# Performance work log

Measured on AMD Instinct MI355X. Metric: run time of the kernel, lower is better.

Reference implementation:

```python
import jax, jax.numpy as jnp
import numpy as np

V = 20000   # token vocab (num_embeddings)
SC = 4000   # sub-char vocab (new_size of sub_char embedding)
D = 128     # embedding_dim
L = 15      # max nodes per decomposition tree (<= 8 leaves)
B, S = 32, 512


def _build_trees(rng):
    """Random binary decomposition trees in topological order (children < parent)."""
    node_ids = np.zeros((V, L), np.int32)
    left = np.full((V, L), -1, np.int32)
    right = np.full((V, L), -1, np.int32)
    last = np.zeros((V,), np.int32)
    for v in range(V):
        n_leaves = int(rng.integers(2, 9))
        stack, nodes = [], []
        leaves_left = n_leaves
        while leaves_left > 0 or len(stack) > 1:
            if leaves_left > 0 and (len(stack) < 2 or rng.random() < 0.5):
                nodes.append((-1, -1)); leaves_left -= 1
            else:
                r = stack.pop(); l = stack.pop()
                nodes.append((l, r))
            stack.append(len(nodes) - 1)
        n = len(nodes)
        for j, (l, r) in enumerate(nodes):
            left[v, j] = l; right[v, j] = r
        node_ids[v, :n] = rng.integers(0, SC, n)
        last[v] = n - 1
    return node_ids, left, right, last


def setup_inputs() -> dict:
    key = jax.random.key(0)
    k1, k2, k3, k4 = jax.random.split(key, 4)
    rng = np.random.default_rng(0)
    node_ids, left, right, last = _build_trees(rng)
    inp = {
        "input": jax.random.randint(k1, (B, S), 0, V, dtype=jnp.int32),
        "node_ids": jnp.asarray(node_ids),
        "left": jnp.asarray(left),
        "right": jnp.asarray(right),
        "last": jnp.asarray(last),
        "emb": jax.random.normal(k2, (SC, 5 * D), jnp.float32) * 0.1,   # sub_char weights
        "Wlh_w": jax.random.normal(k3, (D, 5 * D), jnp.float32) * 0.05,  # Linear(D,5D), x @ W
        "Wlh_b": jnp.zeros((5 * D,), jnp.float32),
        "Wrh_w": jax.random.normal(k4, (D, 5 * D), jnp.float32) * 0.05,
        "Wrh_b": jnp.zeros((5 * D,), jnp.float32),
    }
    return inp


def _tree_lstm(node_ids, left, right, last, emb, Wlh_w, Wlh_b, Wrh_w, Wrh_b):
    nV, nL = node_ids.shape
    gv = jnp.arange(nV)

    def step(carry, xs):
        h_all, c_all = carry                  # [V, L, D] each
        ids, l, r, j = xs                     # [V], [V], [V], scalar
        is_int = (l >= 0)[:, None]            # internal node mask; leaf has l==r==-1
        li, ri = jnp.maximum(l, 0), jnp.maximum(r, 0)
        hl, hr = h_all[gv, li], h_all[gv, ri]  # gather children states [V, D]
        cl, cr = c_all[gv, li], c_all[gv, ri]
        s = emb[ids]                           # [V, 5D]
        s_int = s + (hl @ Wlh_w + Wlh_b) + (hr @ Wrh_w + Wrh_b)
        s = jnp.where(is_int, s_int, s)
        ig, lfg, rfg, og, ug = jnp.split(s, 5, axis=1)
        c = jax.nn.sigmoid(ig) * jnp.tanh(ug)
        c = c + jnp.where(is_int, jax.nn.sigmoid(lfg) * cl + jax.nn.sigmoid(rfg) * cr, 0.0)
        h = jax.nn.sigmoid(og) * jnp.tanh(c)
        h_all = h_all.at[:, j].set(h)
        c_all = c_all.at[:, j].set(c)
        return (h_all, c_all), None

    init = (jnp.zeros((nV, nL, emb.shape[1] // 5), emb.dtype),
            jnp.zeros((nV, nL, emb.shape[1] // 5), emb.dtype))
    xs = (node_ids.T, left.T, right.T, jnp.arange(nL))
    (h_all, _), _ = jax.lax.scan(step, init, xs)
    return h_all[gv, last]                     # root h per vocab entry [V, D]


def reference(input, node_ids, left, right, last, emb, Wlh_w, Wlh_b, Wrh_w, Wrh_b):
    lut = _tree_lstm(node_ids, left, right, last, emb, Wlh_w, Wlh_b, Wrh_w, Wrh_b)  # [V, D]
    return lut[input]                          # [B, S, D]
```

## Files before the change

### kernel.cpp

```cpp
#include <hip/hip_runtime.h>
#include <hip/hip_fp16.h>
#include <math.h>

#define V    20000
#define SCV  4000
#define LL   15
#define OUTN (16384 * 128)

#define LEAF_BIT 0x40000000
#define REF_MASK 0x3FFFFFFF
#define ROOT_BIT 0x20000000
#define SLOT_MASK 0x1FFFFFFF
#define DUMMY_SLOT 89999

#define OFF_COUNTS 0
#define OFF_ROOT   128
#define OFF_LISTS  80384
#define OFF_LEAFH  3920384
#define OFF_LEAFC  5968384
#define OFF_LEAFHH 8016384
#define OFF_LT     9040384
#define OFF_RT     14160384
#define OFF_WT     19280384
#define OFF_BIAS   19608064
#define OFF_HINT   19610624
#define OFF_CINT   65690624
#define OFF_HH     111770624
#define OFF_USED   134810624

__device__ __constant__ int d_listOff[8] = {0, 0, 80000, 120000, 160000, 180000, 200000, 220000};

#define ROUND_BLOCKS 256
#define H1_BLOCKS    1920

typedef _Float16 f16x8 __attribute__((ext_vector_type(8)));
typedef float    f32x4 __attribute__((ext_vector_type(4)));

__device__ __forceinline__ float sigm(float x) { return 1.0f / (1.0f + expf(-x)); }

__global__ void mark_kernel(const int* __restrict__ input, unsigned char* __restrict__ used) {
    int i = blockIdx.x * 256 + threadIdx.x;
    used[input[i]] = 1;
}

__global__ void leaf_kernel(const float* __restrict__ emb,
                            float* __restrict__ leafH, float* __restrict__ leafC,
                            __half* __restrict__ leafHh) {
    int row = blockIdx.x;
    int i   = threadIdx.x;
    const float* e = emb + row * 640;
    float ig = e[i];
    float og = e[384 + i];
    float ug = e[512 + i];
    float c = sigm(ig) * tanhf(ug);
    float h = sigm(og) * tanhf(c);
    leafH[row * 128 + i] = h;
    leafC[row * 128 + i] = c;
    leafHh[row * 128 + i] = __float2half(h);
}

__launch_bounds__(320)
__global__ void table_kernel(const float* __restrict__ leafH,
                             const float* __restrict__ Wl, const float* __restrict__ Wlb,
                             const float* __restrict__ Wr, const float* __restrict__ Wrb,
                             __half* __restrict__ LT, __half* __restrict__ RT) {
    __shared__ float A[16 * 128];
    int which = blockIdx.y;
    const float* W  = which ? Wr : Wl;
    const float* Wb = which ? Wrb : Wlb;
    __half* OUT     = which ? RT : LT;
    int r0 = blockIdx.x * 16;
    int t = threadIdx.x;
    for (int idx = t; idx < 16 * 128; idx += 320) A[idx] = leafH[r0 * 128 + idx];
    float acc0[16], acc1[16];
    float b0 = Wb[2 * t], b1 = Wb[2 * t + 1];
#pragma unroll
    for (int m = 0; m < 16; ++m) { acc0[m] = b0; acc1[m] = b1; }
    __syncthreads();
    const float* Bp = W + 2 * t;
#pragma unroll 1
    for (int kb = 0; kb < 128; kb += 4) {
        float4 a[16];
#pragma unroll
        for (int m = 0; m < 16; ++m) a[m] = *(const float4*)(A + (m << 7) + kb);
        float2 bb[4];
#pragma unroll
        for (int u = 0; u < 4; ++u) bb[u] = *(const float2*)(Bp + (kb + u) * 640);
#pragma unroll
        for (int u = 0; u < 4; ++u)
#pragma unroll
            for (int m = 0; m < 16; ++m) {
                float av = (&a[m].x)[u];
                acc0[m] = fmaf(av, bb[u].x, acc0[m]);
                acc1[m] = fmaf(av, bb[u].y, acc1[m]);
            }
    }
#pragma unroll
    for (int m = 0; m < 16; ++m)
        ((__half2*)OUT)[(r0 + m) * 320 + t] = __float22half2_rn(make_float2(acc0[m], acc1[m]));
}

__global__ void wt_kernel(const float* __restrict__ Wl, const float* __restrict__ Wr,
                          __half* __restrict__ WT) {
    __shared__ float T[64][65];
    int kb = blockIdx.x * 64, nb = blockIdx.y * 64;
    int tx = threadIdx.x & 63, ty = threadIdx.x >> 6;
    for (int kk = ty; kk < 64; kk += 4) {
        int k = kb + kk;
        const float* Wsrc = (k < 128) ? (Wl + k * 640) : (Wr + (k - 128) * 640);
        T[kk][tx] = Wsrc[nb + tx];
    }
    __syncthreads();
    for (int nn = ty; nn < 64; nn += 4)
        WT[(nb + nn) * 256 + kb + tx] = __float2half(T[tx][nn]);
}

__global__ void bias_kernel(const float* __restrict__ Wlb, const float* __restrict__ Wrb,
                            float* __restrict__ biasSum) {
    int i = threadIdx.x;
    biasSum[i] = Wlb[i] + Wrb[i];
}

#define MT 128
__global__ void meta_kernel(const int* __restrict__ node_ids,
                            const int* __restrict__ left,
                            const int* __restrict__ right,
                            const int* __restrict__ last,
                            const unsigned char* __restrict__ used,
                            int* __restrict__ counts,
                            int* __restrict__ rootSlot,
                            int4* __restrict__ lists) {
    __shared__ int  sHei[MT][17];
    __shared__ int  sRef[MT][17];
    __shared__ int4 ebuf[MT][7];
    __shared__ int  ebin[MT][7];
    __shared__ int  locCnt[8];
    __shared__ int  basePos[8];
    __shared__ int  scanBuf[MT];
    __shared__ int  blockBase;

    int tid = threadIdx.x;
    if (tid < 8) locCnt[tid] = 0;
    __syncthreads();

    int v = blockIdx.x * MT + tid;
    int nInt = 0;
    if (v < V && used[v]) {
        int l15[LL], r15[LL], id15[LL];
#pragma unroll
        for (int j = 0; j < LL; ++j) {
            l15[j]  = left[v * LL + j];
            r15[j]  = right[v * LL + j];
            id15[j] = node_ids[v * LL + j];
        }
        int lastv = last[v];
#pragma unroll
        for (int j = 0; j < LL; ++j) {
            if (j <= lastv) {
                int l = l15[j];
                if (l < 0) {
                    sHei[tid][j] = 0;
                    sRef[tid][j] = LEAF_BIT | id15[j];
                } else {
                    int r = r15[j];
                    int hl = sHei[tid][l], hr = sHei[tid][r];
                    int hh = 1 + (hl > hr ? hl : hr);
                    sHei[tid][j] = hh;
                    int pos = atomicAdd(&locCnt[hh], 1);
                    int flag = (j == lastv) ? ROOT_BIT : 0;
                    ebuf[tid][nInt] = make_int4(nInt | flag, id15[j], sRef[tid][l], sRef[tid][r]);
                    ebin[tid][nInt] = (hh << 16) | pos;
                    sRef[tid][j] = nInt;
                    ++nInt;
                }
            }
        }
    }
    scanBuf[tid] = nInt;
    __syncthreads();
    for (int d = 1; d < MT; d <<= 1) {
        int val = (tid >= d) ? scanBuf[tid - d] : 0;
        __syncthreads();
        scanBuf[tid] += val;
        __syncthreads();
    }
    if (tid == 0) blockBase = atomicAdd(&counts[31], scanBuf[MT - 1]);
    if (tid < 8) {
        int c = locCnt[tid];
        basePos[tid] = c ? atomicAdd(&counts[tid], c) : 0;
    }
    __syncthreads();
    int treeBase = blockBase + scanBuf[tid] - nInt;
    if (v < V) rootSlot[v] = treeBase + nInt - 1;
    for (int e = 0; e < nInt; ++e) {
        int4 E  = ebuf[tid][e];
        int md  = ebin[tid][e];
        int hh  = md >> 16, pos = md & 0xFFFF;
        E.x += treeBase;
        E.z = (E.z & LEAF_BIT) ? E.z : (E.z + treeBase);
        E.w = (E.w & LEAF_BIT) ? E.w : (E.w + treeBase);
        lists[d_listOff[hh] + basePos[hh] + pos] = E;
    }
}

__global__ void h1_kernel(const int4* __restrict__ list, const int* __restrict__ cntPtr,
                          const float* __restrict__ emb,
                          const __half* __restrict__ LT, const __half* __restrict__ RT,
                          const float* __restrict__ leafC,
                          float* __restrict__ hInt, float* __restrict__ cInt,
                          __half* __restrict__ hH) {
    int cnt = *cntPtr;
    int j = threadIdx.x & 31;
    for (int n = blockIdx.x * 16 + (threadIdx.x >> 5); n < cnt; n += gridDim.x * 16) {
        int4 E = list[n];
        int li = E.z & REF_MASK, ri = E.w & REF_MASK;
        float4 ev[5]; uint2 lv[5], rv[5];
        const float* eb = emb + E.y * 640 + 4 * j;
        const uint2* lb = (const uint2*)(LT + li * 640) + j;
        const uint2* rb = (const uint2*)(RT + ri * 640) + j;
#pragma unroll
        for (int g = 0; g < 5; ++g) {
            ev[g] = *(const float4*)(eb + g * 128);
            lv[g] = lb[g * 32];
            rv[g] = rb[g * 32];
        }
        float4 cl4 = *(const float4*)(leafC + li * 128 + 4 * j);
        float4 cr4 = *(const float4*)(leafC + ri * 128 + 4 * j);
        float4 co, ho;
#pragma unroll
        for (int u = 0; u < 4; ++u) {
            float s[5];
#pragma unroll
            for (int g = 0; g < 5; ++g) {
                __half2 lh = (u < 2) ? *(__half2*)&lv[g].x : *(__half2*)&lv[g].y;
                __half2 rh = (u < 2) ? *(__half2*)&rv[g].x : *(__half2*)&rv[g].y;
                float lf = (u & 1) ? __high2float(lh) : __low2float(lh);
                float rf = (u & 1) ? __high2float(rh) : __low2float(rh);
                s[g] = (&ev[g].x)[u] + lf + rf;
            }
            float cl = (&cl4.x)[u], cr = (&cr4.x)[u];
            float c = sigm(s[0]) * tanhf(s[4]) + sigm(s[1]) * cl + sigm(s[2]) * cr;
            float h = sigm(s[3]) * tanhf(c);
            (&co.x)[u] = c; (&ho.x)[u] = h;
        }
        int slot = E.x & SLOT_MASK;
        if (E.x & ROOT_BIT) {
            *(float4*)(hInt + slot * 128 + 4 * j) = ho;
        } else {
            *(float4*)(cInt + slot * 128 + 4 * j) = co;
            __half2 h0 = __float22half2_rn(make_float2(ho.x, ho.y));
            __half2 h1v = __float22half2_rn(make_float2(ho.z, ho.w));
            uint2 hp; hp.x = *(unsigned int*)&h0; hp.y = *(unsigned int*)&h1v;
            *(uint2*)(hH + slot * 128 + 4 * j) = hp;
        }
    }
}

__launch_bounds__(512, 2)
__global__ void round_mfma(const int4* __restrict__ list, const int* __restrict__ cntPtr,
                           const float* __restrict__ emb, const __half* __restrict__ WT,
                           const float* __restrict__ biasSum,
                           const __half* __restrict__ leafHh, const float* __restrict__ leafC,
                           float* __restrict__ hInt, float* __restrict__ cInt,
                           __half* __restrict__ hH) {
    __shared__ __half Ah[64][264];
    __shared__ int4 meta[64];
    int cnt = *cntPtr;
    int nGroups = (cnt + 63) >> 6;
    int t = threadIdx.x;
    int lane = t & 63, wave = t >> 6;
    int ln15 = lane & 15, quad = lane >> 4;
    for (int grp = blockIdx.x; grp < nGroups; grp += gridDim.x) {
        int base = grp * 64;
        int rows = cnt - base; if (rows > 64) rows = 64;
        if (t < 64) {
            int4 E;
            if (t < rows) E = list[base + t];
            else { E.x = DUMMY_SLOT; E.y = 0; E.z = LEAF_BIT; E.w = LEAF_BIT; }
            meta[t] = E;
        }
        __syncthreads();
#pragma unroll
        for (int it = 0; it < 4; ++it) {
            int idx = t + it * 512;
            int m = idx >> 5, q = idx & 31;
            int ref = (q < 16) ? meta[m].z : meta[m].w;
            const __half* hs = (ref & LEAF_BIT) ? leafHh : hH;
            uint4 v = *(const uint4*)(hs + (ref & REF_MASK) * 128 + (q & 15) * 8);
            *(uint4*)(&Ah[m][q * 8]) = v;
        }
        float bs[5];
#pragma unroll
        for (int p = 0; p < 5; ++p) bs[p] = biasSum[p * 128 + 16 * wave + ln15];
        f32x4 acc[4][5];
#pragma unroll
        for (int c = 0; c < 4; ++c)
#pragma unroll
            for (int r = 0; r < 4; ++r) {
                const float* eb = emb + meta[c * 16 + quad * 4 + r].y * 640 + 16 * wave + ln15;
#pragma unroll
                for (int p = 0; p < 5; ++p)
                    acc[c][p][r] = eb[p * 128] + bs[p];
            }
        __syncthreads();
        const __half* wbase = WT + (16 * wave + ln15) * 256 + quad * 8;
#pragma unroll 2
        for (int kb = 0; kb < 8; ++kb) {
            f16x8 bf[5];
#pragma unroll
            for (int p = 0; p < 5; ++p)
                bf[p] = *(const f16x8*)((const void*)(wbase + p * 32768 + kb * 32));
            f16x8 af[4];
#pragma unroll
            for (int c = 0; c < 4; ++c)
                af[c] = *(const f16x8*)((const void*)&Ah[c * 16 + ln15][kb * 32 + quad * 8]);
#pragma unroll
            for (int p = 0; p < 5; ++p)
#pragma unroll
                for (int c = 0; c < 4; ++c)
                    acc[c][p] = __builtin_amdgcn_mfma_f32_16x16x32_f16(af[c], bf[p], acc[c][p], 0, 0, 0);
        }
        int d = 16 * wave + ln15;
#pragma unroll
        for (int c = 0; c < 4; ++c)
#pragma unroll
            for (int r = 0; r < 4; ++r) {
                int4 E = meta[c * 16 + quad * 4 + r];
                float ig = acc[c][0][r], lfg = acc[c][1][r], rfg = acc[c][2][r];
                float og = acc[c][3][r], ug = acc[c][4][r];
                float cl = ((E.z & LEAF_BIT) ? leafC : cInt)[(E.z & REF_MASK) * 128 + d];
                float cr = ((E.w & LEAF_BIT) ? leafC : cInt)[(E.w & REF_MASK) * 128 + d];
                float cc = sigm(ig) * tanhf(ug) + sigm(lfg) * cl + sigm(rfg) * cr;
                float hh = sigm(og) * tanhf(cc);
                int slot = E.x & SLOT_MASK;
                if (E.x & ROOT_BIT) {
                    hInt[slot * 128 + d] = hh;
                } else {
                    cInt[slot * 128 + d] = cc;
                    hH[slot * 128 + d] = __float2half(hh);
                }
            }
        __syncthreads();
    }
}

__global__ void gather_kernel(const int* __restrict__ input,
                              const int* __restrict__ rootSlot,
                              const float* __restrict__ hInt,
                              float4* __restrict__ out) {
    int idx = blockIdx.x * 256 + threadIdx.x;
    int token = input[idx >> 5];
    int d = idx & 31;
    out[idx] = ((const float4*)hInt)[rootSlot[token] * 32 + d];
}

extern "C" void kernel_launch(void* const* d_in, const int* in_sizes, int n_in,
                              void* d_out, int out_size, void* d_ws, size_t ws_size,
                              hipStream_t stream) {
    const int*   input    = (const int*)d_in[0];
    const int*   node_ids = (const int*)d_in[1];
    const int*   left     = (const int*)d_in[2];
    const int*   right    = (const int*)d_in[3];
    const int*   last     = (const int*)d_in[4];
    const float* emb      = (const float*)d_in[5];
    const float* Wl       = (const float*)d_in[6];
    const float* Wlb      = (const float*)d_in[7];
    const float* Wr       = (const float*)d_in[8];
    const float* Wrb      = (const float*)d_in[9];
    float* out = (float*)d_out;

    char* ws = (char*)d_ws;
    int*    counts   = (int*)(ws + OFF_COUNTS);
    int*    rootSlot = (int*)(ws + OFF_ROOT);
    int4*   lists    = (int4*)(ws + OFF_LISTS);
    float*  leafH    = (float*)(ws + OFF_LEAFH);
    float*  leafC    = (float*)(ws + OFF_LEAFC);
    __half* leafHh   = (__half*)(ws + OFF_LEAFHH);
    __half* LTp      = (__half*)(ws + OFF_LT);
    __half* RTp      = (__half*)(ws + OFF_RT);
    __half* WT       = (__half*)(ws + OFF_WT);
    float*  biasSum  = (float*)(ws + OFF_BIAS);
    float*  hInt     = (float*)(ws + OFF_HINT);
    float*  cInt     = (float*)(ws + OFF_CINT);
    __half* hH       = (__half*)(ws + OFF_HH);
    unsigned char* usedp = (unsigned char*)(ws + OFF_USED);

    (void)hipMemsetAsync(counts, 0, 128, stream);
    (void)hipMemsetAsync(usedp, 0, V, stream);

    mark_kernel<<<64, 256, 0, stream>>>(input, usedp);
    leaf_kernel<<<SCV, 128, 0, stream>>>(emb, leafH, leafC, leafHh);
    table_kernel<<<dim3(SCV / 16, 2), 320, 0, stream>>>(leafH, Wl, Wlb, Wr, Wrb, LTp, RTp);
    wt_kernel<<<dim3(4, 10), 256, 0, stream>>>(Wl, Wr, WT);
    bias_kernel<<<1, 640, 0, stream>>>(Wlb, Wrb, biasSum);
    meta_kernel<<<(V + MT - 1) / MT, MT, 0, stream>>>(node_ids, left, right, last, usedp,
                                                      counts, rootSlot, lists);

    h1_kernel<<<H1_BLOCKS, 512, 0, stream>>>(lists, counts + 1, emb, LTp, RTp, leafC,
                                             hInt, cInt, hH);

    static const int h_listOff[8] = {0, 0, 80000, 120000, 160000, 180000, 200000, 220000};
    for (int h = 2; h <= 7; ++h) {
        round_mfma<<<ROUND_BLOCKS, 512, 0, stream>>>(
            lists + h_listOff[h], counts + h,
            emb, WT, biasSum, leafHh, leafC, hInt, cInt, hH);
    }

    gather_kernel<<<OUTN / 4 / 256, 256, 0, stream>>>(input, rootSlot, hInt, (float4*)out);
}
```

Measured before the change: 291.7 us.

## Fuse all tree-LSTM stages into one persistent kernel with grid barriers

Replaces the chain of about eleven kernel launches with a single persistent kernel of 256 blocks. It runs leaf precompute, used-marking, weight transpose, metadata bucketing, every height level and the final gather, separated by atomic-counter grid barriers. The precomputed left/right leaf projection tables and the separate height-1 path are dropped, so height-1 nodes now go through the same MFMA path and leaf rows are computed as part of the GEMM. This removes per-launch overhead and the leaf-table GEMM. In exchange it relies on all 256 blocks being co-resident and adds spin-wait barriers, and the meta stage only uses 157 of 256 blocks with 128 of 512 threads.

```diff
diff --git a/kernel.cpp b/kernel.cpp
--- a/kernel.cpp
+++ b/kernel.cpp
@@ -16,11 +16,8 @@
 #define OFF_COUNTS 0
 #define OFF_ROOT   128
 #define OFF_LISTS  80384
-#define OFF_LEAFH  3920384
 #define OFF_LEAFC  5968384
 #define OFF_LEAFHH 8016384
-#define OFF_LT     9040384
-#define OFF_RT     14160384
 #define OFF_WT     19280384
 #define OFF_BIAS   19608064
 #define OFF_HINT   19610624
@@ -30,328 +27,247 @@
 
 __device__ __constant__ int d_listOff[8] = {0, 0, 80000, 120000, 160000, 180000, 200000, 220000};
 
-#define ROUND_BLOCKS 256
-#define H1_BLOCKS    1920
+#define FBLK 256
+#define FT   512
+#define MT   128
 
 typedef _Float16 f16x8 __attribute__((ext_vector_type(8)));
 typedef float    f32x4 __attribute__((ext_vector_type(4)));
 
 __device__ __forceinline__ float sigm(float x) { return 1.0f / (1.0f + expf(-x)); }
 
-__global__ void mark_kernel(const int* __restrict__ input, unsigned char* __restrict__ used) {
-    int i = blockIdx.x * 256 + threadIdx.x;
-    used[input[i]] = 1;
+union SharedU {
+    struct { __half Ah[64][264]; int4 meta[64]; } f;
+    struct { float T[64][65]; } w;
+    struct {
+        int  sHei[MT][17];
+        int  sRef[MT][17];
+        int4 ebuf[MT][7];
+        int  ebin[MT][7];
+        int  locCnt[8];
+        int  basePos[8];
+        int  scanBuf[MT];
+        int  blockBase;
+    } m;
+};
+
+__device__ __forceinline__ void grid_barrier(int* bar) {
+    __syncthreads();
+    if (threadIdx.x == 0) {
+        __threadfence();
+        __hip_atomic_fetch_add(bar, 1, __ATOMIC_RELEASE, __HIP_MEMORY_SCOPE_AGENT);
+        while (__hip_atomic_load(bar, __ATOMIC_ACQUIRE, __HIP_MEMORY_SCOPE_AGENT) < (int)gridDim.x)
+            __builtin_amdgcn_s_sleep(2);
+        __threadfence();
+    }
+    __syncthreads();
 }
 
-__global__ void leaf_kernel(const float* __restrict__ emb,
-                            float* __restrict__ leafH, float* __restrict__ leafC,
-                            __half* __restrict__ leafHh) {
-    int row = blockIdx.x;
-    int i   = threadIdx.x;
-    const float* e = emb + row * 640;
-    float ig = e[i];
-    float og = e[384 + i];
-    float ug = e[512 + i];
-    float c = sigm(ig) * tanhf(ug);
-    float h = sigm(og) * tanhf(c);
-    leafH[row * 128 + i] = h;
-    leafC[row * 128 + i] = c;
-    leafHh[row * 128 + i] = __float2half(h);
-}
-
-__launch_bounds__(320)
-__global__ void table_kernel(const float* __restrict__ leafH,
-                             const float* __restrict__ Wl, const float* __restrict__ Wlb,
-                             const float* __restrict__ Wr, const float* __restrict__ Wrb,
-                             __half* __restrict__ LT, __half* __restrict__ RT) {
-    __shared__ float A[16 * 128];
-    int which = blockIdx.y;
-    const float* W  = which ? Wr : Wl;
-    const float* Wb = which ? Wrb : Wlb;
-    __half* OUT     = which ? RT : LT;
-    int r0 = blockIdx.x * 16;
+__launch_bounds__(FT, 2)
+__global__ void forest_kernel(const int* __restrict__ input,
+                              const int* __restrict__ node_ids,
+                              const int* __restrict__ left,
+                              const int* __restrict__ right,
+                              const int* __restrict__ last,
+                              const float* __restrict__ emb,
+                              const float* __restrict__ Wl, const float* __restrict__ Wlb,
+                              const float* __restrict__ Wr, const float* __restrict__ Wrb,
+                              int* counts, int* rootSlot, int4* lists,
+                              float* leafC, __half* leafHh,
+                              __half* WT, float* biasSum,
+                              float* hInt, float* cInt, __half* hH,
+                              unsigned char* used, float4* out) {
+    __shared__ SharedU S;
     int t = threadIdx.x;
-    for (int idx = t; idx < 16 * 128; idx += 320) A[idx] = leafH[r0 * 128 + idx];
-    float acc0[16], acc1[16];
-    float b0 = Wb[2 * t], b1 = Wb[2 * t + 1];
-#pragma unroll
-    for (int m = 0; m < 16; ++m) { acc0[m] = b0; acc1[m] = b1; }
-    __syncthreads();
-    const float* Bp = W + 2 * t;
-#pragma unroll 1
-    for (int kb = 0; kb < 128; kb += 4) {
-        float4 a[16];
-#pragma unroll
-        for (int m = 0; m < 16; ++m) a[m] = *(const float4*)(A + (m << 7) + kb);
-        float2 bb[4];
-#pragma unroll
-        for (int u = 0; u < 4; ++u) bb[u] = *(const float2*)(Bp + (kb + u) * 640);
-#pragma unroll
-        for (int u = 0; u < 4; ++u)
-#pragma unroll
-            for (int m = 0; m < 16; ++m) {
-                float av = (&a[m].x)[u];
-                acc0[m] = fmaf(av, bb[u].x, acc0[m]);
-                acc1[m] = fmaf(av, bb[u].y, acc1[m]);
-            }
-    }
-#pragma unroll
-    for (int m = 0; m < 16; ++m)
-        ((__half2*)OUT)[(r0 + m) * 320 + t] = __float22half2_rn(make_float2(acc0[m], acc1[m]));
-}
-
-__global__ void wt_kernel(const float* __restrict__ Wl, const float* __restrict__ Wr,
-                          __half* __restrict__ WT) {
-    __shared__ float T[64][65];
-    int kb = blockIdx.x * 64, nb = blockIdx.y * 64;
-    int tx = threadIdx.x & 63, ty = threadIdx.x >> 6;
-    for (int kk = ty; kk < 64; kk += 4) {
-        int k = kb + kk;
-        const float* Wsrc = (k < 128) ? (Wl + k * 640) : (Wr + (k - 128) * 640);
-        T[kk][tx] = Wsrc[nb + tx];
-    }
-    __syncthreads();
-    for (int nn = ty; nn < 64; nn += 4)
-        WT[(nb + nn) * 256 + kb + tx] = __float2half(T[tx][nn]);
-}
-
-__global__ void bias_kernel(const float* __restrict__ Wlb, const float* __restrict__ Wrb,
-                            float* __restrict__ biasSum) {
-    int i = threadIdx.x;
-    biasSum[i] = Wlb[i] + Wrb[i];
-}
-
-#define MT 128
-__global__ void meta_kernel(const int* __restrict__ node_ids,
-                            const int* __restrict__ left,
-                            const int* __restrict__ right,
-                            const int* __restrict__ last,
-                            const unsigned char* __restrict__ used,
-                            int* __restrict__ counts,
-                            int* __restrict__ rootSlot,
-                            int4* __restrict__ lists) {
-    __shared__ int  sHei[MT][17];
-    __shared__ int  sRef[MT][17];
-    __shared__ int4 ebuf[MT][7];
-    __shared__ int  ebin[MT][7];
-    __shared__ int  locCnt[8];
-    __shared__ int  basePos[8];
-    __shared__ int  scanBuf[MT];
-    __shared__ int  blockBase;
-
-    int tid = threadIdx.x;
-    if (tid < 8) locCnt[tid] = 0;
-    __syncthreads();
-
-    int v = blockIdx.x * MT + tid;
-    int nInt = 0;
-    if (v < V && used[v]) {
-        int l15[LL], r15[LL], id15[LL];
-#pragma unroll
-        for (int j = 0; j < LL; ++j) {
-            l15[j]  = left[v * LL + j];
-            r15[j]  = right[v * LL + j];
-            id15[j] = node_ids[v * LL + j];
-        }
-        int lastv = last[v];
-#pragma unroll
-        for (int j = 0; j < LL; ++j) {
-            if (j <= lastv) {
-                int l = l15[j];
-                if (l < 0) {
-                    sHei[tid][j] = 0;
-                    sRef[tid][j] = LEAF_BIT | id15[j];
-                } else {
-                    int r = r15[j];
-                    int hl = sHei[tid][l], hr = sHei[tid][r];
-                    int hh = 1 + (hl > hr ? hl : hr);
-                    sHei[tid][j] = hh;
-                    int pos = atomicAdd(&locCnt[hh], 1);
-                    int flag = (j == lastv) ? ROOT_BIT : 0;
-                    ebuf[tid][nInt] = make_int4(nInt | flag, id15[j], sRef[tid][l], sRef[tid][r]);
-                    ebin[tid][nInt] = (hh << 16) | pos;
-                    sRef[tid][j] = nInt;
-                    ++nInt;
+    int* bar = counts + 16;
+
+    for (int r = blockIdx.x * 4 + (t >> 7); r < SCV; r += gridDim.x * 4) {
+        int i = t & 127;
+        const float* e = emb + r * 640;
+        float c = sigm(e[i]) * tanhf(e[512 + i]);
+        float h = sigm(e[384 + i]) * tanhf(c);
+        leafC[r * 128 + i] = c;
+        leafHh[r * 128 + i] = __float2half(h);
+    }
+    for (int i = blockIdx.x * FT + t; i < 16384; i += gridDim.x * FT)
+        used[input[i]] = 1;
+    if (blockIdx.x == 40)
+        for (int i = t; i < 640; i += FT) biasSum[i] = Wlb[i] + Wrb[i];
+    for (int tile = blockIdx.x; tile < 40; tile += gridDim.x) {
+        int kb = (tile & 3) * 64, nb = (tile >> 2) * 64;
+        int tx = t & 63, ty = (t >> 6) & 3;
+        if (t < 256) {
+            for (int kk = ty; kk < 64; kk += 4) {
+                int k = kb + kk;
+                const float* Wsrc = (k < 128) ? (Wl + k * 640) : (Wr + (k - 128) * 640);
+                S.w.T[kk][tx] = Wsrc[nb + tx];
+            }
+        }
+        __syncthreads();
+        if (t < 256) {
+            for (int nn = ty; nn < 64; nn += 4)
+                WT[(nb + nn) * 256 + kb + tx] = __float2half(S.w.T[tx][nn]);
+        }
+        __syncthreads();
+    }
+    grid_barrier(&bar[0]);
+
+    {
+        int tile = blockIdx.x;
+        bool act = (tile * MT) < V;
+        if (t < 8) S.m.locCnt[t] = 0;
+        __syncthreads();
+        int v = tile * MT + t;
+        int nInt = 0;
+        if (act && t < MT && v < V && used[v]) {
+            int l15[LL], r15[LL], id15[LL];
+#pragma unroll
+            for (int j = 0; j < LL; ++j) {
+                l15[j]  = left[v * LL + j];
+                r15[j]  = right[v * LL + j];
+                id15[j] = node_ids[v * LL + j];
+            }
+            int lastv = last[v];
+#pragma unroll
+            for (int j = 0; j < LL; ++j) {
+                if (j <= lastv) {
+                    int l = l15[j];
+                    if (l < 0) {
+                        S.m.sHei[t][j] = 0;
+                        S.m.sRef[t][j] = LEAF_BIT | id15[j];
+                    } else {
+                        int r = r15[j];
+                        int hl = S.m.sHei[t][l], hr = S.m.sHei[t][r];
+                        int hh = 1 + (hl > hr ? hl : hr);
+                        S.m.sHei[t][j] = hh;
+                        int pos = atomicAdd(&S.m.locCnt[hh], 1);
+                        int flag = (j == lastv) ? ROOT_BIT : 0;
+                        S.m.ebuf[t][nInt] = make_int4(nInt | flag, id15[j],
+                                                      S.m.sRef[t][l], S.m.sRef[t][r]);
+                        S.m.ebin[t][nInt] = (hh << 16) | pos;
+                        S.m.sRef[t][j] = nInt;
+                        ++nInt;
+                    }
                 }
             }
         }
-    }
-    scanBuf[tid] = nInt;
-    __syncthreads();
-    for (int d = 1; d < MT; d <<= 1) {
-        int val = (tid >= d) ? scanBuf[tid - d] : 0;
-        __syncthreads();
-        scanBuf[tid] += val;
-        __syncthreads();
-    }
-    if (tid == 0) blockBase = atomicAdd(&counts[31], scanBuf[MT - 1]);
-    if (tid < 8) {
-        int c = locCnt[tid];
-        basePos[tid] = c ? atomicAdd(&counts[tid], c) : 0;
-    }
-    __syncthreads();
-    int treeBase = blockBase + scanBuf[tid] - nInt;
-    if (v < V) rootSlot[v] = treeBase + nInt - 1;
-    for (int e = 0; e < nInt; ++e) {
-        int4 E  = ebuf[tid][e];
-        int md  = ebin[tid][e];
-        int hh  = md >> 16, pos = md & 0xFFFF;
-        E.x += treeBase;
-        E.z = (E.z & LEAF_BIT) ? E.z : (E.z + treeBase);
-        E.w = (E.w & LEAF_BIT) ? E.w : (E.w + treeBase);
-        lists[d_listOff[hh] + basePos[hh] + pos] = E;
-    }
-}
-
-__global__ void h1_kernel(const int4* __restrict__ list, const int* __restrict__ cntPtr,
-                          const float* __restrict__ emb,
-                          const __half* __restrict__ LT, const __half* __restrict__ RT,
-                          const float* __restrict__ leafC,
-                          float* __restrict__ hInt, float* __restrict__ cInt,
-                          __half* __restrict__ hH) {
-    int cnt = *cntPtr;
-    int j = threadIdx.x & 31;
-    for (int n = blockIdx.x * 16 + (threadIdx.x >> 5); n < cnt; n += gridDim.x * 16) {
-        int4 E = list[n];
-        int li = E.z & REF_MASK, ri = E.w & REF_MASK;
-        float4 ev[5]; uint2 lv[5], rv[5];
-        const float* eb = emb + E.y * 640 + 4 * j;
-        const uint2* lb = (const uint2*)(LT + li * 640) + j;
-        const uint2* rb = (const uint2*)(RT + ri * 640) + j;
-#pragma unroll
-        for (int g = 0; g < 5; ++g) {
-            ev[g] = *(const float4*)(eb + g * 128);
-            lv[g] = lb[g * 32];
-            rv[g] = rb[g * 32];
-        }
-        float4 cl4 = *(const float4*)(leafC + li * 128 + 4 * j);
-        float4 cr4 = *(const float4*)(leafC + ri * 128 + 4 * j);
-        float4 co, ho;
-#pragma unroll
-        for (int u = 0; u < 4; ++u) {
-            float s[5];
-#pragma unroll
-            for (int g = 0; g < 5; ++g) {
-                __half2 lh = (u < 2) ? *(__half2*)&lv[g].x : *(__half2*)&lv[g].y;
-                __half2 rh = (u < 2) ? *(__half2*)&rv[g].x : *(__half2*)&rv[g].y;
-                float lf = (u & 1) ? __high2float(lh) : __low2float(lh);
-                float rf = (u & 1) ? __high2float(rh) : __low2float(rh);
-                s[g] = (&ev[g].x)[u] + lf + rf;
-            }
-            float cl = (&cl4.x)[u], cr = (&cr4.x)[u];
-            float c = sigm(s[0]) * tanhf(s[4]) + sigm(s[1]) * cl + sigm(s[2]) * cr;
-            float h = sigm(s[3]) * tanhf(c);
-            (&co.x)[u] = c; (&ho.x)[u] = h;
-        }
-        int slot = E.x & SLOT_MASK;
-        if (E.x & ROOT_BIT) {
-            *(float4*)(hInt + slot * 128 + 4 * j) = ho;
-        } else {
-            *(float4*)(cInt + slot * 128 + 4 * j) = co;
-            __half2 h0 = __float22half2_rn(make_float2(ho.x, ho.y));
-            __half2 h1v = __float22half2_rn(make_float2(ho.z, ho.w));
-            uint2 hp; hp.x = *(unsigned int*)&h0; hp.y = *(unsigned int*)&h1v;
-            *(uint2*)(hH + slot * 128 + 4 * j) = hp;
-        }
-    }
-}
-
-__launch_bounds__(512, 2)
-__global__ void round_mfma(const int4* __restrict__ list, const int* __restrict__ cntPtr,
-                           const float* __restrict__ emb, const __half* __restrict__ WT,
-                           const float* __restrict__ biasSum,
-                           const __half* __restrict__ leafHh, const float* __restrict__ leafC,
-                           float* __restrict__ hInt, float* __restrict__ cInt,
-                           __half* __restrict__ hH) {
-    __shared__ __half Ah[64][264];
-    __shared__ int4 meta[64];
-    int cnt = *cntPtr;
-    int nGroups = (cnt + 63) >> 6;
-    int t = threadIdx.x;
+        if (t < MT) S.m.scanBuf[t] = nInt;
+        __syncthreads();
+        for (int d = 1; d < MT; d <<= 1) {
+            int val = (t >= d && t < MT) ? S.m.scanBuf[t - d] : 0;
+            __syncthreads();
+            if (t < MT) S.m.scanBuf[t] += val;
+            __syncthreads();
+        }
+        if (act && t == 0) S.m.blockBase = atomicAdd(&counts[31], S.m.scanBuf[MT - 1]);
+        if (act && t < 8) {
+            int c = S.m.locCnt[t];
+            S.m.basePos[t] = c ? atomicAdd(&counts[t], c) : 0;
+        }
+        __syncthreads();
+        if (act && t < MT) {
+            int treeBase = S.m.blockBase + S.m.scanBuf[t] - nInt;
+            if (nInt > 0 && v < V) rootSlot[v] = treeBase + nInt - 1;
+            for (int e = 0; e < nInt; ++e) {
+                int4 E  = S.m.ebuf[t][e];
+                int md  = S.m.ebin[t][e];
+                int hh  = md >> 16, pos = md & 0xFFFF;
+                E.x += treeBase;
+                E.z = (E.z & LEAF_BIT) ? E.z : (E.z + treeBase);
+                E.w = (E.w & LEAF_BIT) ? E.w : (E.w + treeBase);
+                lists[d_listOff[hh] + S.m.basePos[hh] + pos] = E;
+            }
+        }
+    }
+    grid_barrier(&bar[1]);
+
     int lane = t & 63, wave = t >> 6;
     int ln15 = lane & 15, quad = lane >> 4;
-    for (int grp = blockIdx.x; grp < nGroups; grp += gridDim.x) {
-        int base = grp * 64;
-        int rows = cnt - base; if (rows > 64) rows = 64;
-        if (t < 64) {
-            int4 E;
-            if (t < rows) E = list[base + t];
-            else { E.x = DUMMY_SLOT; E.y = 0; E.z = LEAF_BIT; E.w = LEAF_BIT; }
-            meta[t] = E;
-        }
-        __syncthreads();
-#pragma unroll
-        for (int it = 0; it < 4; ++it) {
-            int idx = t + it * 512;
-            int m = idx >> 5, q = idx & 31;
-            int ref = (q < 16) ? meta[m].z : meta[m].w;
-            const __half* hs = (ref & LEAF_BIT) ? leafHh : hH;
-            uint4 v = *(const uint4*)(hs + (ref & REF_MASK) * 128 + (q & 15) * 8);
-            *(uint4*)(&Ah[m][q * 8]) = v;
-        }
-        float bs[5];
-#pragma unroll
-        for (int p = 0; p < 5; ++p) bs[p] = biasSum[p * 128 + 16 * wave + ln15];
-        f32x4 acc[4][5];
-#pragma unroll
-        for (int c = 0; c < 4; ++c)
-#pragma unroll
-            for (int r = 0; r < 4; ++r) {
-                const float* eb = emb + meta[c * 16 + quad * 4 + r].y * 640 + 16 * wave + ln15;
+    for (int h = 1; h <= 7; ++h) {
+        int cnt = counts[h];
+        const int4* list = lists + d_listOff[h];
+        int nGroups = (cnt + 63) >> 6;
+        for (int grp = blockIdx.x; grp < nGroups; grp += gridDim.x) {
+            int base = grp * 64;
+            int rows = cnt - base; if (rows > 64) rows = 64;
+            if (t < 64) {
+                int4 E;
+                if (t < rows) E = list[base + t];
+                else { E.x = DUMMY_SLOT; E.y = 0; E.z = LEAF_BIT; E.w = LEAF_BIT; }
+                S.f.meta[t] = E;
+            }
+            __syncthreads();
+#pragma unroll
+            for (int it = 0; it < 4; ++it) {
+                int idx = t + it * FT;
+                int m = idx >> 5, q = idx & 31;
+                int ref = (q < 16) ? S.f.meta[m].z : S.f.meta[m].w;
+                const __half* hs = (ref & LEAF_BIT) ? leafHh : hH;
+                uint4 vv = *(const uint4*)(hs + (ref & REF_MASK) * 128 + (q & 15) * 8);
+                *(uint4*)(&S.f.Ah[m][q * 8]) = vv;
+            }
+            float bs[5];
+#pragma unroll
+            for (int p = 0; p < 5; ++p) bs[p] = biasSum[p * 128 + 16 * wave + ln15];
+            f32x4 acc[4][5];
+#pragma unroll
+            for (int c = 0; c < 4; ++c)
+#pragma unroll
+                for (int r = 0; r < 4; ++r) {
+                    const float* eb = emb + S.f.meta[c * 16 + quad * 4 + r].y * 640
+                                          + 16 * wave + ln15;
+#pragma unroll
+                    for (int p = 0; p < 5; ++p)
+                        acc[c][p][r] = eb[p * 128] + bs[p];
+                }
+            __syncthreads();
+            const __half* wbase = WT + (16 * wave + ln15) * 256 + quad * 8;
+#pragma unroll 2
+            for (int kb = 0; kb < 8; ++kb) {
+                f16x8 bf[5];
 #pragma unroll
                 for (int p = 0; p < 5; ++p)
-                    acc[c][p][r] = eb[p * 128] + bs[p];
-            }
-        __syncthreads();
-        const __half* wbase = WT + (16 * wave + ln15) * 256 + quad * 8;
-#pragma unroll 2
-        for (int kb = 0; kb < 8; ++kb) {
-            f16x8 bf[5];
-#pragma unroll
-            for (int p = 0; p < 5; ++p)
-                bf[p] = *(const f16x8*)((const void*)(wbase + p * 32768 + kb * 32));
-            f16x8 af[4];
+                    bf[p] = *(const f16x8*)((const void*)(wbase + p * 32768 + kb * 32));
+                f16x8 af[4];
+#pragma unroll
+                for (int c = 0; c < 4; ++c)
+                    af[c] = *(const f16x8*)((const void*)&S.f.Ah[c * 16 + ln15][kb * 32 + quad * 8]);
+#pragma unroll
+                for (int p = 0; p < 5; ++p)
+#pragma unroll
+                    for (int c = 0; c < 4; ++c)
+                        acc[c][p] = __builtin_amdgcn_mfma_f32_16x16x32_f16(af[c], bf[p], acc[c][p], 0, 0, 0);
+            }
+            int d = 16 * wave + ln15;
 #pragma unroll
             for (int c = 0; c < 4; ++c)
-                af[c] = *(const f16x8*)((const void*)&Ah[c * 16 + ln15][kb * 32 + quad * 8]);
-#pragma unroll
-            for (int p = 0; p < 5; ++p)
-#pragma unroll
-                for (int c = 0; c < 4; ++c)
-                    acc[c][p] = __builtin_amdgcn_mfma_f32_16x16x32_f16(af[c], bf[p], acc[c][p], 0, 0, 0);
-        }
-        int d = 16 * wave + ln15;
-#pragma unroll
-        for (int c = 0; c < 4; ++c)
-#pragma unroll
-            for (int r = 0; r < 4; ++r) {
-                int4 E = meta[c * 16 + quad * 4 + r];
-                float ig = acc[c][0][r], lfg = acc[c][1][r], rfg = acc[c][2][r];
-                float og = acc[c][3][r], ug = acc[c][4][r];
-                float cl = ((E.z & LEAF_BIT) ? leafC : cInt)[(E.z & REF_MASK) * 128 + d];
-                float cr = ((E.w & LEAF_BIT) ? leafC : cInt)[(E.w & REF_MASK) * 128 + d];
-                float cc = sigm(ig) * tanhf(ug) + sigm(lfg) * cl + sigm(rfg) * cr;
-                float hh = sigm(og) * tanhf(cc);
-                int slot = E.x & SLOT_MASK;
-                if (E.x & ROOT_BIT) {
-                    hInt[slot * 128 + d] = hh;
-                } else {
-                    cInt[slot * 128 + d] = cc;
-                    hH[slot * 128 + d] = __float2half(hh);
+#pragma unroll
+                for (int r = 0; r < 4; ++r) {
+                    int4 E = S.f.meta[c * 16 + quad * 4 + r];
+                    float ig = acc[c][0][r], lfg = acc[c][1][r], rfg = acc[c][2][r];
+                    float og = acc[c][3][r], ug = acc[c][4][r];
+                    float cl = ((E.z & LEAF_BIT) ? leafC : cInt)[(E.z & REF_MASK) * 128 + d];
+                    float cr = ((E.w & LEAF_BIT) ? leafC : cInt)[(E.w & REF_MASK) * 128 + d];
+                    float cc = sigm(ig) * tanhf(ug) + sigm(lfg) * cl + sigm(rfg) * cr;
+                    float hh2 = sigm(og) * tanhf(cc);
+                    int slot = E.x & SLOT_MASK;
+                    if (E.x & ROOT_BIT) {
+                        hInt[slot * 128 + d] = hh2;
+                    } else {
+                        cInt[slot * 128 + d] = cc;
+                        hH[slot * 128 + d] = __float2half(hh2);
+                    }
                 }
-            }
-        __syncthreads();
-    }
-}
-
-__global__ void gather_kernel(const int* __restrict__ input,
-                              const int* __restrict__ rootSlot,
-                              const float* __restrict__ hInt,
-                              float4* __restrict__ out) {
-    int idx = blockIdx.x * 256 + threadIdx.x;
-    int token = input[idx >> 5];
-    int d = idx & 31;
-    out[idx] = ((const float4*)hInt)[rootSlot[token] * 32 + d];
+            __syncthreads();
+        }
+        grid_barrier(&bar[2 + (h - 1)]);
+    }
+
+    for (int idx = blockIdx.x * FT + t; idx < OUTN / 4; idx += gridDim.x * FT) {
+        int token = input[idx >> 5];
+        int d = idx & 31;
+        out[idx] = ((const float4*)hInt)[rootSlot[token] * 32 + d];
+    }
 }
 
 extern "C" void kernel_launch(void* const* d_in, const int* in_sizes, int n_in,
@@ -373,11 +289,8 @@
     int*    counts   = (int*)(ws + OFF_COUNTS);
     int*    rootSlot = (int*)(ws + OFF_ROOT);
     int4*   lists    = (int4*)(ws + OFF_LISTS);
-    float*  leafH    = (float*)(ws + OFF_LEAFH);
     float*  leafC    = (float*)(ws + OFF_LEAFC);
     __half* leafHh   = (__half*)(ws + OFF_LEAFHH);
-    __half* LTp      = (__half*)(ws + OFF_LT);
-    __half* RTp      = (__half*)(ws + OFF_RT);
     __half* WT       = (__half*)(ws + OFF_WT);
     float*  biasSum  = (float*)(ws + OFF_BIAS);
     float*  hInt     = (float*)(ws + OFF_HINT);
@@ -388,23 +301,9 @@
     (void)hipMemsetAsync(counts, 0, 128, stream);
     (void)hipMemsetAsync(usedp, 0, V, stream);
 
-    mark_kernel<<<64, 256, 0, stream>>>(input, usedp);
-    leaf_kernel<<<SCV, 128, 0, stream>>>(emb, leafH, leafC, leafHh);
-    table_kernel<<<dim3(SCV / 16, 2), 320, 0, stream>>>(leafH, Wl, Wlb, Wr, Wrb, LTp, RTp);
-    wt_kernel<<<dim3(4, 10), 256, 0, stream>>>(Wl, Wr, WT);
-    bias_kernel<<<1, 640, 0, stream>>>(Wlb, Wrb, biasSum);
-    meta_kernel<<<(V + MT - 1) / MT, MT, 0, stream>>>(node_ids, left, right, last, usedp,
-                                                      counts, rootSlot, lists);
-
-    h1_kernel<<<H1_BLOCKS, 512, 0, stream>>>(lists, counts + 1, emb, LTp, RTp, leafC,
-                                             hInt, cInt, hH);
-
-    static const int h_listOff[8] = {0, 0, 80000, 120000, 160000, 180000, 200000, 220000};
-    for (int h = 2; h <= 7; ++h) {
-        round_mfma<<<ROUND_BLOCKS, 512, 0, stream>>>(
-            lists + h_listOff[h], counts + h,
-            emb, WT, biasSum, leafHh, leafC, hInt, cInt, hH);
-    }
-
-    gather_kernel<<<OUTN / 4 / 256, 256, 0, stream>>>(input, rootSlot, hInt, (float4*)out);
+    forest_kernel<<<FBLK, FT, 0, stream>>>(input, node_ids, left, right, last,
+                                           emb, Wl, Wlb, Wr, Wrb,
+                                           counts, rootSlot, lists, leafC, leafHh,
+                                           WT, biasSum, hInt, cInt, hH,
+                                           usedp, (float4*)out);
 }
```

Measured after the change: 1.029 ms. 3.53x slower.

## Fuse prep kernels, drop leaf LUT tables, run height-1 via MFMA rounds

Applied to the files above, without the earlier changes.

Merges the mark, leaf, weight-transpose and bias kernels into one prep kernel. It removes the precomputed per-leaf left/right projection tables (table_kernel) and the specialised h1 kernel, so height-1 nodes now go through the generic MFMA round kernel. It also sizes each round's grid to that height's expected work. This cuts launch count and the large leaf-table GEMM at the cost of doing those projections inside the height-1 round, and adds a guard so rootSlot is only written for trees with internal nodes.

```diff
diff --git a/kernel.cpp b/kernel.cpp
--- a/kernel.cpp
+++ b/kernel.cpp
@@ -16,11 +16,8 @@
 #define OFF_COUNTS 0
 #define OFF_ROOT   128
 #define OFF_LISTS  80384
-#define OFF_LEAFH  3920384
 #define OFF_LEAFC  5968384
 #define OFF_LEAFHH 8016384
-#define OFF_LT     9040384
-#define OFF_RT     14160384
 #define OFF_WT     19280384
 #define OFF_BIAS   19608064
 #define OFF_HINT   19610624
@@ -30,98 +27,48 @@
 
 __device__ __constant__ int d_listOff[8] = {0, 0, 80000, 120000, 160000, 180000, 200000, 220000};
 
-#define ROUND_BLOCKS 256
-#define H1_BLOCKS    1920
+#define MT 128
 
 typedef _Float16 f16x8 __attribute__((ext_vector_type(8)));
 typedef float    f32x4 __attribute__((ext_vector_type(4)));
 
 __device__ __forceinline__ float sigm(float x) { return 1.0f / (1.0f + expf(-x)); }
 
-__global__ void mark_kernel(const int* __restrict__ input, unsigned char* __restrict__ used) {
-    int i = blockIdx.x * 256 + threadIdx.x;
-    used[input[i]] = 1;
-}
-
-__global__ void leaf_kernel(const float* __restrict__ emb,
-                            float* __restrict__ leafH, float* __restrict__ leafC,
-                            __half* __restrict__ leafHh) {
-    int row = blockIdx.x;
-    int i   = threadIdx.x;
-    const float* e = emb + row * 640;
-    float ig = e[i];
-    float og = e[384 + i];
-    float ug = e[512 + i];
-    float c = sigm(ig) * tanhf(ug);
-    float h = sigm(og) * tanhf(c);
-    leafH[row * 128 + i] = h;
-    leafC[row * 128 + i] = c;
-    leafHh[row * 128 + i] = __float2half(h);
-}
-
-__launch_bounds__(320)
-__global__ void table_kernel(const float* __restrict__ leafH,
-                             const float* __restrict__ Wl, const float* __restrict__ Wlb,
-                             const float* __restrict__ Wr, const float* __restrict__ Wrb,
-                             __half* __restrict__ LT, __half* __restrict__ RT) {
-    __shared__ float A[16 * 128];
-    int which = blockIdx.y;
-    const float* W  = which ? Wr : Wl;
-    const float* Wb = which ? Wrb : Wlb;
-    __half* OUT     = which ? RT : LT;
-    int r0 = blockIdx.x * 16;
-    int t = threadIdx.x;
-    for (int idx = t; idx < 16 * 128; idx += 320) A[idx] = leafH[r0 * 128 + idx];
-    float acc0[16], acc1[16];
-    float b0 = Wb[2 * t], b1 = Wb[2 * t + 1];
-#pragma unroll
-    for (int m = 0; m < 16; ++m) { acc0[m] = b0; acc1[m] = b1; }
-    __syncthreads();
-    const float* Bp = W + 2 * t;
-#pragma unroll 1
-    for (int kb = 0; kb < 128; kb += 4) {
-        float4 a[16];
-#pragma unroll
-        for (int m = 0; m < 16; ++m) a[m] = *(const float4*)(A + (m << 7) + kb);
-        float2 bb[4];
-#pragma unroll
-        for (int u = 0; u < 4; ++u) bb[u] = *(const float2*)(Bp + (kb + u) * 640);
-#pragma unroll
-        for (int u = 0; u < 4; ++u)
-#pragma unroll
-            for (int m = 0; m < 16; ++m) {
-                float av = (&a[m].x)[u];
-                acc0[m] = fmaf(av, bb[u].x, acc0[m]);
-                acc1[m] = fmaf(av, bb[u].y, acc1[m]);
-            }
-    }
-#pragma unroll
-    for (int m = 0; m < 16; ++m)
-        ((__half2*)OUT)[(r0 + m) * 320 + t] = __float22half2_rn(make_float2(acc0[m], acc1[m]));
-}
-
-__global__ void wt_kernel(const float* __restrict__ Wl, const float* __restrict__ Wr,
-                          __half* __restrict__ WT) {
+__global__ void prep_kernel(const int* __restrict__ input,
+                            const float* __restrict__ emb,
+                            const float* __restrict__ Wl, const float* __restrict__ Wlb,
+                            const float* __restrict__ Wr, const float* __restrict__ Wrb,
+                            float* __restrict__ leafC, __half* __restrict__ leafHh,
+                            __half* __restrict__ WT, float* __restrict__ biasSum,
+                            unsigned char* __restrict__ used) {
     __shared__ float T[64][65];
-    int kb = blockIdx.x * 64, nb = blockIdx.y * 64;
-    int tx = threadIdx.x & 63, ty = threadIdx.x >> 6;
-    for (int kk = ty; kk < 64; kk += 4) {
-        int k = kb + kk;
-        const float* Wsrc = (k < 128) ? (Wl + k * 640) : (Wr + (k - 128) * 640);
-        T[kk][tx] = Wsrc[nb + tx];
-    }
-    __syncthreads();
-    for (int nn = ty; nn < 64; nn += 4)
-        WT[(nb + nn) * 256 + kb + tx] = __float2half(T[tx][nn]);
-}
-
-__global__ void bias_kernel(const float* __restrict__ Wlb, const float* __restrict__ Wrb,
-                            float* __restrict__ biasSum) {
-    int i = threadIdx.x;
-    biasSum[i] = Wlb[i] + Wrb[i];
-}
-
-#define MT 128
+    int t = threadIdx.x, bid = blockIdx.x;
+    for (int r = bid * 2 + (t >> 7); r < SCV; r += gridDim.x * 2) {
+        int i = t & 127;
+        const float* e = emb + r * 640;
+        float c = sigm(e[i]) * tanhf(e[512 + i]);
+        float h = sigm(e[384 + i]) * tanhf(c);
+        leafC[r * 128 + i] = c;
+        leafHh[r * 128 + i] = __float2half(h);
+    }
+    for (int i = bid * 256 + t; i < 16384; i += gridDim.x * 256)
+        used[input[i]] = 1;
+    if (bid == 41)
+        for (int i = t; i < 640; i += 256) biasSum[i] = Wlb[i] + Wrb[i];
+    if (bid < 40) {
+        int kb = (bid & 3) * 64, nb = (bid >> 2) * 64;
+        int tx = t & 63, ty = t >> 6;
+        for (int kk = ty; kk < 64; kk += 4) {
+            int k = kb + kk;
+            const float* Wsrc = (k < 128) ? (Wl + k * 640) : (Wr + (k - 128) * 640);
+            T[kk][tx] = Wsrc[nb + tx];
+        }
+        __syncthreads();
+        for (int nn = ty; nn < 64; nn += 4)
+            WT[(nb + nn) * 256 + kb + tx] = __float2half(T[tx][nn]);
+    }
+}
+
 __global__ void meta_kernel(const int* __restrict__ node_ids,
                             const int* __restrict__ left,
                             const int* __restrict__ right,
@@ -191,7 +138,7 @@
     }
     __syncthreads();
     int treeBase = blockBase + scanBuf[tid] - nInt;
-    if (v < V) rootSlot[v] = treeBase + nInt - 1;
+    if (v < V && nInt > 0) rootSlot[v] = treeBase + nInt - 1;
     for (int e = 0; e < nInt; ++e) {
         int4 E  = ebuf[tid][e];
         int md  = ebin[tid][e];
@@ -200,59 +147,6 @@
         E.z = (E.z & LEAF_BIT) ? E.z : (E.z + treeBase);
         E.w = (E.w & LEAF_BIT) ? E.w : (E.w + treeBase);
         lists[d_listOff[hh] + basePos[hh] + pos] = E;
-    }
-}
-
-__global__ void h1_kernel(const int4* __restrict__ list, const int* __restrict__ cntPtr,
-                          const float* __restrict__ emb,
-                          const __half* __restrict__ LT, const __half* __restrict__ RT,
-                          const float* __restrict__ leafC,
-                          float* __restrict__ hInt, float* __restrict__ cInt,
-                          __half* __restrict__ hH) {
-    int cnt = *cntPtr;
-    int j = threadIdx.x & 31;
-    for (int n = blockIdx.x * 16 + (threadIdx.x >> 5); n < cnt; n += gridDim.x * 16) {
-        int4 E = list[n];
-        int li = E.z & REF_MASK, ri = E.w & REF_MASK;
-        float4 ev[5]; uint2 lv[5], rv[5];
-        const float* eb = emb + E.y * 640 + 4 * j;
-        const uint2* lb = (const uint2*)(LT + li * 640) + j;
-        const uint2* rb = (const uint2*)(RT + ri * 640) + j;
-#pragma unroll
-        for (int g = 0; g < 5; ++g) {
-            ev[g] = *(const float4*)(eb + g * 128);
-            lv[g] = lb[g * 32];
-            rv[g] = rb[g * 32];
-        }
-        float4 cl4 = *(const float4*)(leafC + li * 128 + 4 * j);
-        float4 cr4 = *(const float4*)(leafC + ri * 128 + 4 * j);
-        float4 co, ho;
-#pragma unroll
-        for (int u = 0; u < 4; ++u) {
-            float s[5];
-#pragma unroll
-            for (int g = 0; g < 5; ++g) {
-                __half2 lh = (u < 2) ? *(__half2*)&lv[g].x : *(__half2*)&lv[g].y;
-                __half2 rh = (u < 2) ? *(__half2*)&rv[g].x : *(__half2*)&rv[g].y;
-                float lf = (u & 1) ? __high2float(lh) : __low2float(lh);
-                float rf = (u & 1) ? __high2float(rh) : __low2float(rh);
-                s[g] = (&ev[g].x)[u] + lf + rf;
-            }
-            float cl = (&cl4.x)[u], cr = (&cr4.x)[u];
-            float c = sigm(s[0]) * tanhf(s[4]) + sigm(s[1]) * cl + sigm(s[2]) * cr;
-            float h = sigm(s[3]) * tanhf(c);
-            (&co.x)[u] = c; (&ho.x)[u] = h;
-        }
-        int slot = E.x & SLOT_MASK;
-        if (E.x & ROOT_BIT) {
-            *(float4*)(hInt + slot * 128 + 4 * j) = ho;
-        } else {
-            *(float4*)(cInt + slot * 128 + 4 * j) = co;
-            __half2 h0 = __float22half2_rn(make_float2(ho.x, ho.y));
-            __half2 h1v = __float22half2_rn(make_float2(ho.z, ho.w));
-            uint2 hp; hp.x = *(unsigned int*)&h0; hp.y = *(unsigned int*)&h1v;
-            *(uint2*)(hH + slot * 128 + 4 * j) = hp;
-        }
     }
 }
 
@@ -331,13 +225,13 @@
                 float cl = ((E.z & LEAF_BIT) ? leafC : cInt)[(E.z & REF_MASK) * 128 + d];
                 float cr = ((E.w & LEAF_BIT) ? leafC : cInt)[(E.w & REF_MASK) * 128 + d];
                 float cc = sigm(ig) * tanhf(ug) + sigm(lfg) * cl + sigm(rfg) * cr;
-                float hh = sigm(og) * tanhf(cc);
+                float hh2 = sigm(og) * tanhf(cc);
                 int slot = E.x & SLOT_MASK;
                 if (E.x & ROOT_BIT) {
-                    hInt[slot * 128 + d] = hh;
+                    hInt[slot * 128 + d] = hh2;
                 } else {
                     cInt[slot * 128 + d] = cc;
-                    hH[slot * 128 + d] = __float2half(hh);
+                    hH[slot * 128 + d] = __float2half(hh2);
                 }
             }
         __syncthreads();
@@ -373,11 +267,8 @@
     int*    counts   = (int*)(ws + OFF_COUNTS);
     int*    rootSlot = (int*)(ws + OFF_ROOT);
     int4*   lists    = (int4*)(ws + OFF_LISTS);
-    float*  leafH    = (float*)(ws + OFF_LEAFH);
     float*  leafC    = (float*)(ws + OFF_LEAFC);
     __half* leafHh   = (__half*)(ws + OFF_LEAFHH);
-    __half* LTp      = (__half*)(ws + OFF_LT);
-    __half* RTp      = (__half*)(ws + OFF_RT);
     __half* WT       = (__half*)(ws + OFF_WT);
     float*  biasSum  = (float*)(ws + OFF_BIAS);
     float*  hInt     = (float*)(ws + OFF_HINT);
@@ -388,20 +279,15 @@
     (void)hipMemsetAsync(counts, 0, 128, stream);
     (void)hipMemsetAsync(usedp, 0, V, stream);
 
-    mark_kernel<<<64, 256, 0, stream>>>(input, usedp);
-    leaf_kernel<<<SCV, 128, 0, stream>>>(emb, leafH, leafC, leafHh);
-    table_kernel<<<dim3(SCV / 16, 2), 320, 0, stream>>>(leafH, Wl, Wlb, Wr, Wrb, LTp, RTp);
-    wt_kernel<<<dim3(4, 10), 256, 0, stream>>>(Wl, Wr, WT);
-    bias_kernel<<<1, 640, 0, stream>>>(Wlb, Wrb, biasSum);
+    prep_kernel<<<1024, 256, 0, stream>>>(input, emb, Wl, Wlb, Wr, Wrb,
+                                          leafC, leafHh, WT, biasSum, usedp);
     meta_kernel<<<(V + MT - 1) / MT, MT, 0, stream>>>(node_ids, left, right, last, usedp,
                                                       counts, rootSlot, lists);
 
-    h1_kernel<<<H1_BLOCKS, 512, 0, stream>>>(lists, counts + 1, emb, LTp, RTp, leafC,
-                                             hInt, cInt, hH);
-
     static const int h_listOff[8] = {0, 0, 80000, 120000, 160000, 180000, 200000, 220000};
-    for (int h = 2; h <= 7; ++h) {
-        round_mfma<<<ROUND_BLOCKS, 512, 0, stream>>>(
+    static const int h_grid[8]    = {0, 512, 512, 256, 128, 32, 8, 4};
+    for (int h = 1; h <= 7; ++h) {
+        round_mfma<<<h_grid[h], 512, 0, stream>>>(
             lists + h_listOff[h], counts + h,
             emb, WT, biasSum, leafHh, leafC, hInt, cInt, hH);
     }
```

After: 334.1 us. +14.6%, slower.
